# Kernel tuning notes

Measured on AMD Instinct MI355X. Metric: run time of the kernel, lower is better.

Reference implementation:

```python
import jax, jax.numpy as jnp
import numpy as np

NUM_NODES = 100000
NUM_EDGES = 1600000
EMB, HID, IN = 32, 64, 128


def gcn_conv(x, W, b, src, dst, n):
    # PyG GCNConv: add self-loops, symmetric normalization, linear transform, sum-aggregate, bias.
    h = x @ W                                   # [n, out]
    deg = jnp.zeros((n,), x.dtype).at[dst].add(1.0) + 1.0  # degree incl. self-loop
    dinv = jax.lax.rsqrt(deg)                   # deg^{-1/2}
    norm = dinv[src] * dinv[dst]                # [E]
    msg = h[src] * norm[:, None]                # gather + scale  [E, out]
    agg = jax.ops.segment_sum(msg, dst, num_segments=n)
    agg = agg + h * (dinv * dinv)[:, None]      # self-loop contribution
    return agg + b


def setup_inputs() -> dict:
    key = jax.random.key(0)
    ks = jax.random.split(key, 10)
    f32 = jnp.float32
    edge_index = jax.random.randint(ks[0], (2, NUM_EDGES), 0, NUM_NODES, dtype=jnp.int64 if jax.config.jax_enable_x64 else jnp.int32)
    def glorot(k, fan_in, fan_out):
        s = (6.0 / (fan_in + fan_out)) ** 0.5
        return jax.random.uniform(k, (fan_in, fan_out), f32, -s, s)
    return {
        'edge_index': edge_index,
        'embedding': jax.random.normal(ks[1], (NUM_NODES, EMB), f32),
        'We1': glorot(ks[2], EMB, HID), 'be1': jnp.zeros((HID,), f32),
        'We2': glorot(ks[3], HID, EMB), 'be2': jnp.zeros((EMB,), f32),
        'Wd1': glorot(ks[4], EMB, HID), 'bd1': jnp.zeros((HID,), f32),
        'Wd2': glorot(ks[5], HID, IN),  'bd2': jnp.zeros((IN,), f32),
    }


def reference(edge_index, embedding, We1, be1, We2, be2, Wd1, bd1, Wd2, bd2):
    src, dst = edge_index[0], edge_index[1]
    n = NUM_NODES
    # encoder
    x = jax.nn.relu(gcn_conv(embedding, We1, be1, src, dst, n))
    z = jax.nn.relu(gcn_conv(x, We2, be2, src, dst, n))
    # decoder
    y = jax.nn.relu(gcn_conv(z, Wd1, bd1, src, dst, n))
    recon_x = gcn_conv(y, Wd2, bd2, src, dst, n)
    return (recon_x, z)
```

## Files before the change

kernel.cpp:

```cpp
#include <hip/hip_runtime.h>
#include <hip/hip_fp16.h>

#define NN 100000
#define NE 1600000
#define NB 782
#define EPB 8192
#define NBLK_A 196
#define SCNT (NB * NBLK_A)
#define SC_NB ((SCNT + 1023) / 1024)
#define CAP 4096


__global__ void bhistA_kernel(const int* __restrict__ dst, int* __restrict__ histT) {
    __shared__ int hist[NB];
    int t = threadIdx.x, b = blockIdx.x;
    for (int i = t; i < NB; i += 256) hist[i] = 0;
    __syncthreads();
    int e0 = b * EPB;
    for (int i = t; i < EPB; i += 256) {
        int e = e0 + i;
        if (e < NE) atomicAdd(&hist[dst[e] >> 7], 1);
    }
    __syncthreads();
    for (int i = t; i < NB; i += 256) histT[i * NBLK_A + b] = hist[i];
}

__global__ void scan1g_kernel(const int* __restrict__ in, int* __restrict__ out,
                              int* __restrict__ blkSum) {
    __shared__ int ts[256];
    int t = threadIdx.x, b = blockIdx.x;
    int base = b * 1024 + t * 4;
    int4 c = {0, 0, 0, 0};
    if (base < SCNT) c = *(const int4*)(in + base);
    int s = c.x + c.y + c.z + c.w;
    ts[t] = s;
    __syncthreads();
    for (int ofs = 1; ofs < 256; ofs <<= 1) {
        int v = (t >= ofs) ? ts[t - ofs] : 0;
        __syncthreads();
        ts[t] += v;
        __syncthreads();
    }
    if (t == 255) blkSum[b] = ts[255];
    int ex = ts[t] - s;
    if (base < SCNT) {
        int4 p;
        p.x = ex; p.y = ex + c.x; p.z = p.y + c.y; p.w = p.z + c.z;
        *(int4*)(out + base) = p;
    }
}

__global__ void scan2g_kernel(int* __restrict__ blkSum) {
    __shared__ int ts[256];
    int t = threadIdx.x;
    int v = (t < SC_NB) ? blkSum[t] : 0;
    ts[t] = v;
    __syncthreads();
    for (int ofs = 1; ofs < 256; ofs <<= 1) {
        int u = (t >= ofs) ? ts[t - ofs] : 0;
        __syncthreads();
        ts[t] += u;
        __syncthreads();
    }
    if (t < SC_NB) blkSum[t] = ts[t] - v;
}

__global__ void scan3g_kernel(int* __restrict__ out, const int* __restrict__ blkSum) {
    int b = blockIdx.x;
    int base = b * 1024 + threadIdx.x * 4;
    int off = blkSum[b];
    if (base < SCNT) {
        int4 p = *(const int4*)(out + base);
        p.x += off; p.y += off; p.z += off; p.w += off;
        *(int4*)(out + base) = p;
    }
}

__global__ void bscatB_kernel(const int* __restrict__ src, const int* __restrict__ dst,
                              const int* __restrict__ scanT, int2* __restrict__ ebuf) {
    __shared__ int cur[NB];
    int t = threadIdx.x, b = blockIdx.x;
    for (int i = t; i < NB; i += 256) cur[i] = scanT[i * NBLK_A + b];
    __syncthreads();
    int e0 = b * EPB;
    for (int i = t; i < EPB; i += 256) {
        int e = e0 + i;
        if (e < NE) {
            int d = dst[e];
            int p = atomicAdd(&cur[d >> 7], 1);
            ebuf[p] = make_int2(src[e], d);
        }
    }
}

__global__ void csrC_kernel(const int2* __restrict__ ebuf, const int* __restrict__ scanT,
                            int* __restrict__ row_ptr, int* __restrict__ col,
                            float* __restrict__ dinv) {
    __shared__ int2 es[CAP];
    __shared__ int hist[128];
    __shared__ int ts[128];
    __shared__ int cur[128];
    int t = threadIdx.x, b = blockIdx.x;
    int base = scanT[b * NBLK_A];
    int end  = (b + 1 < NB) ? scanT[(b + 1) * NBLK_A] : NE;
    int cnt = end - base;
    if (t < 128) hist[t] = 0;
    __syncthreads();
    for (int i = t; i < cnt; i += 256) {
        int2 e = ebuf[base + i];
        if (i < CAP) es[i] = e;
        atomicAdd(&hist[e.y & 127], 1);
    }
    __syncthreads();
    if (t < 128) ts[t] = hist[t];
    __syncthreads();
    for (int ofs = 1; ofs < 128; ofs <<= 1) {
        int v = 0;
        if (t < 128 && t >= ofs) v = ts[t - ofs];
        __syncthreads();
        if (t < 128) ts[t] += v;
        __syncthreads();
    }
    if (t < 128) {
        int ex = ts[t] - hist[t];
        cur[t] = ex;
        int g = b * 128 + t;
        if (g < NN) {
            row_ptr[g] = base + ex;
            dinv[g] = rsqrtf((float)hist[t] + 1.0f);
        }
    }
    if (b == 0 && t == 0) row_ptr[NN] = NE;
    __syncthreads();
    for (int i = t; i < cnt; i += 256) {
        int2 e = (i < CAP) ? es[i] : ebuf[base + i];
        int r = atomicAdd(&cur[e.y & 127], 1);
        col[base + r] = e.x;
    }
}


__device__ inline ushort4 f4_to_h4(float4 v) {
    ushort4 o;
    o.x = __half_as_ushort(__float2half(v.x));
    o.y = __half_as_ushort(__float2half(v.y));
    o.z = __half_as_ushort(__float2half(v.z));
    o.w = __half_as_ushort(__float2half(v.w));
    return o;
}

template<int C>
__global__ void quant_kernel(const float4* __restrict__ x, const float* __restrict__ dinv,
                             ushort4* __restrict__ q) {
    constexpr int TPN = C / 4;
    int gid = blockIdx.x * blockDim.x + threadIdx.x;
    if (gid >= NN * TPN) return;
    int node = gid / TPN;
    float d = dinv[node];
    float4 v = x[gid];
    v.x *= d; v.y *= d; v.z *= d; v.w *= d;
    q[gid] = f4_to_h4(v);
}

template<int IN, int OUT, bool RELU, bool HASBIAS, bool QUANT>
__global__ void mm_kernel(const float* __restrict__ x, const float* __restrict__ W,
                          const float* __restrict__ bias, const float* __restrict__ dinv,
                          float4* __restrict__ out, ushort4* __restrict__ qout) {
    constexpr int CG   = OUT / 4;
    constexpr int RG   = 256 / CG;
    constexpr int ROWS = RG * 4;
    constexpr int P    = IN + 4;
    __shared__ float4 Ws[IN * CG];
    __shared__ float  xs[ROWS * P];

    int tid = threadIdx.x;
    const float4* W4 = (const float4*)W;
    for (int i = tid; i < IN * CG; i += 256) Ws[i] = W4[i];

    int n0 = blockIdx.x * ROWS;
    for (int i = tid; i < ROWS * IN; i += 256) {
        int r = i / IN, c = i & (IN - 1);
        size_t g = (size_t)n0 * IN + i;
        if (g < (size_t)NN * IN) xs[r * P + c] = x[g];
    }
    __syncthreads();

    int cg = tid % CG;
    int rg = tid / CG;

    float4 acc[4] = {{0,0,0,0},{0,0,0,0},{0,0,0,0},{0,0,0,0}};
#pragma unroll 2
    for (int k = 0; k < IN; k += 4) {
        float4 w0 = Ws[(k + 0) * CG + cg];
        float4 w1 = Ws[(k + 1) * CG + cg];
        float4 w2 = Ws[(k + 2) * CG + cg];
        float4 w3 = Ws[(k + 3) * CG + cg];
#pragma unroll
        for (int i = 0; i < 4; ++i) {
            float4 xq = *(const float4*)&xs[(i * RG + rg) * P + k];
            acc[i].x = fmaf(xq.x, w0.x, acc[i].x);
            acc[i].y = fmaf(xq.x, w0.y, acc[i].y);
            acc[i].z = fmaf(xq.x, w0.z, acc[i].z);
            acc[i].w = fmaf(xq.x, w0.w, acc[i].w);
            acc[i].x = fmaf(xq.y, w1.x, acc[i].x);
            acc[i].y = fmaf(xq.y, w1.y, acc[i].y);
            acc[i].z = fmaf(xq.y, w1.z, acc[i].z);
            acc[i].w = fmaf(xq.y, w1.w, acc[i].w);
            acc[i].x = fmaf(xq.z, w2.x, acc[i].x);
            acc[i].y = fmaf(xq.z, w2.y, acc[i].y);
            acc[i].z = fmaf(xq.z, w2.z, acc[i].z);
            acc[i].w = fmaf(xq.z, w2.w, acc[i].w);
            acc[i].x = fmaf(xq.w, w3.x, acc[i].x);
            acc[i].y = fmaf(xq.w, w3.y, acc[i].y);
            acc[i].z = fmaf(xq.w, w3.z, acc[i].z);
            acc[i].w = fmaf(xq.w, w3.w, acc[i].w);
        }
    }

    float4 bb = {0, 0, 0, 0};
    if (HASBIAS) bb = ((const float4*)bias)[cg];
#pragma unroll
    for (int i = 0; i < 4; ++i) {
        int node = n0 + i * RG + rg;
        if (node >= NN) continue;
        float4 r = acc[i];
        if (HASBIAS) { r.x += bb.x; r.y += bb.y; r.z += bb.z; r.w += bb.w; }
        if (RELU) {
            r.x = fmaxf(r.x, 0.f); r.y = fmaxf(r.y, 0.f);
            r.z = fmaxf(r.z, 0.f); r.w = fmaxf(r.w, 0.f);
        }
        if (QUANT) {
            float d = dinv[node];
            r.x *= d; r.y *= d; r.z *= d; r.w *= d;
            qout[(size_t)node * CG + cg] = f4_to_h4(r);
        } else {
            out[(size_t)node * CG + cg] = r;
        }
    }
}


__device__ inline void acc8(float* a, uint4 u) {
    const __half2* hp = (const __half2*)&u;
#pragma unroll
    for (int q = 0; q < 4; ++q) {
        float2 f = __half22float2(hp[q]);
        a[2 * q]     += f.x;
        a[2 * q + 1] += f.y;
    }
}

template<int C, bool BIASRELU, bool WRITE_Q>
__global__ void agg_kernel(const uint4* __restrict__ h, const int* __restrict__ row_ptr,
                           const int* __restrict__ col, const float* __restrict__ dinv,
                           const float* __restrict__ b, float4* __restrict__ out,
                           uint4* __restrict__ qout) {
    constexpr int TPN = C / 8;
    int gid = blockIdx.x * blockDim.x + threadIdx.x;
    int node = gid / TPN;
    int cg = gid % TPN;
    if (node >= NN) return;
    int beg = row_ptr[node];
    int end = row_ptr[node + 1];

    float a[8] = {0, 0, 0, 0, 0, 0, 0, 0};
    acc8(a, h[(size_t)node * TPN + cg]);

    int j = beg;
    for (; j + 4 <= end; j += 4) {
        int s0 = col[j], s1 = col[j + 1], s2 = col[j + 2], s3 = col[j + 3];
        uint4 u0 = h[(size_t)s0 * TPN + cg];
        uint4 u1 = h[(size_t)s1 * TPN + cg];
        uint4 u2 = h[(size_t)s2 * TPN + cg];
        uint4 u3 = h[(size_t)s3 * TPN + cg];
        acc8(a, u0); acc8(a, u1); acc8(a, u2); acc8(a, u3);
    }
    for (; j < end; ++j) acc8(a, h[(size_t)col[j] * TPN + cg]);

    float d = dinv[node];
    float r[8];
    if (BIASRELU) {
        const float* bp = b + cg * 8;
#pragma unroll
        for (int q = 0; q < 8; ++q) r[q] = fmaxf(fmaf(d, a[q], bp[q]), 0.f);
    } else {
#pragma unroll
        for (int q = 0; q < 8; ++q) r[q] = d * a[q];
    }
    float4* op = out + (size_t)node * (C / 4) + cg * 2;
    op[0] = make_float4(r[0], r[1], r[2], r[3]);
    op[1] = make_float4(r[4], r[5], r[6], r[7]);
    if (WRITE_Q) {
        uint4 qv;
        __half2* qp = (__half2*)&qv;
#pragma unroll
        for (int q = 0; q < 4; ++q)
            qp[q] = __float22half2_rn(make_float2(r[2 * q] * d, r[2 * q + 1] * d));
        qout[(size_t)node * TPN + cg] = qv;
    }
}


extern "C" void kernel_launch(void* const* d_in, const int* in_sizes, int n_in,
                              void* d_out, int out_size, void* d_ws, size_t ws_size,
                              hipStream_t stream) {
    const int* ei = (const int*)d_in[0];
    const int* src = ei;
    const int* dst = ei + NE;
    const float* emb = (const float*)d_in[1];
    const float* We1 = (const float*)d_in[2]; const float* be1 = (const float*)d_in[3];
    const float* We2 = (const float*)d_in[4]; const float* be2 = (const float*)d_in[5];
    const float* Wd1 = (const float*)d_in[6]; const float* bd1 = (const float*)d_in[7];
    const float* Wd2 = (const float*)d_in[8]; const float* bd2 = (const float*)d_in[9];

    float* outp  = (float*)d_out;
    float* recon = outp;
    float* z     = outp + (size_t)NN * 128;

    char* ws = (char*)d_ws;
    size_t off = 0;
    auto alloc = [&](size_t bytes) {
        void* p = ws + off;
        off += (bytes + 255) & ~(size_t)255;
        return p;
    };
    int*     row_ptr = (int*)    alloc((size_t)(NN + 1) * 4);
    int*     col     = (int*)    alloc((size_t)NE * 4);
    float*   dinv    = (float*)  alloc((size_t)NN * 4);
    int*     histT   = (int*)    alloc((size_t)SCNT * 4);
    int*     scanT   = (int*)    alloc((size_t)SCNT * 4);
    int*     blkSum  = (int*)    alloc((size_t)SC_NB * 4);
    void*    region1 = alloc((size_t)NE * 8);
    ushort4* qA      = (ushort4*)alloc((size_t)NN * 64 * 2);
    ushort4* qB      = (ushort4*)alloc((size_t)NN * 64 * 2);
    float*   fB      = (float*)  alloc((size_t)NN * 64 * 4);
    int2*    ebuf    = (int2*)region1;
    float*   fA      = (float*)region1;
    (void)ws_size; (void)in_sizes; (void)n_in; (void)out_size;

    bhistA_kernel<<<NBLK_A, 256, 0, stream>>>(dst, histT);
    scan1g_kernel<<<SC_NB, 256, 0, stream>>>(histT, scanT, blkSum);
    scan2g_kernel<<<1, 256, 0, stream>>>(blkSum);
    scan3g_kernel<<<SC_NB, 256, 0, stream>>>(scanT, blkSum);
    bscatB_kernel<<<NBLK_A, 256, 0, stream>>>(src, dst, scanT, ebuf);
    csrC_kernel<<<NB, 256, 0, stream>>>(ebuf, scanT, row_ptr, col, dinv);

    quant_kernel<32><<<(NN * 8 + 255) / 256, 256, 0, stream>>>((const float4*)emb, dinv, qA);
    agg_kernel<32, false, false><<<(NN * 4 + 255) / 256, 256, 0, stream>>>(
        (const uint4*)qA, row_ptr, col, dinv, nullptr, (float4*)fA, nullptr);
    mm_kernel<32, 64, true, true, false><<<(NN + 63) / 64, 256, 0, stream>>>(
        fA, We1, be1, dinv, (float4*)fB, nullptr);

    mm_kernel<64, 32, false, false, true><<<(NN + 127) / 128, 256, 0, stream>>>(
        fB, We2, nullptr, dinv, nullptr, qB);
    agg_kernel<32, true, true><<<(NN * 4 + 255) / 256, 256, 0, stream>>>(
        (const uint4*)qB, row_ptr, col, dinv, be2, (float4*)z, (uint4*)qA);

    agg_kernel<32, false, false><<<(NN * 4 + 255) / 256, 256, 0, stream>>>(
        (const uint4*)qA, row_ptr, col, dinv, nullptr, (float4*)fA, nullptr);
    mm_kernel<32, 64, true, true, true><<<(NN + 63) / 64, 256, 0, stream>>>(
        fA, Wd1, bd1, dinv, nullptr, qB);

    agg_kernel<64, false, false><<<(NN * 8 + 255) / 256, 256, 0, stream>>>(
        (const uint4*)qB, row_ptr, col, dinv, nullptr, (float4*)fB, nullptr);
    mm_kernel<64, 128, false, true, false><<<(NN + 31) / 32, 256, 0, stream>>>(
        fB, Wd2, bd2, dinv, (float4*)recon, nullptr);
}
```

Baseline: 260.2 us.

## Pack edge bucket entries into one int, add blocks, unroll gathers by eight

Edges in the bucket buffer are now packed into a single 32-bit word, with the source in the low 20 bits and the local destination row in the high bits, instead of an int2. This halves the scatter and CSR-build traffic and the shared-memory staging footprint. The histogram and scatter passes use four times more blocks with fewer edges each, which grows the transposed histogram, so the second scan stage moves to 1024 threads. The aggregation kernel gains an 8-wide gather loop to keep more loads in flight, at the cost of more registers.

```diff
diff --git a/kernel.cpp b/kernel.cpp
--- a/kernel.cpp
+++ b/kernel.cpp
@@ -4,8 +4,8 @@
 #define NN 100000
 #define NE 1600000
 #define NB 782
-#define EPB 8192
-#define NBLK_A 196
+#define EPB 2048
+#define NBLK_A 782
 #define SCNT (NB * NBLK_A)
 #define SC_NB ((SCNT + 1023) / 1024)
 #define CAP 4096
@@ -51,12 +51,12 @@
 }
 
 __global__ void scan2g_kernel(int* __restrict__ blkSum) {
-    __shared__ int ts[256];
+    __shared__ int ts[1024];
     int t = threadIdx.x;
     int v = (t < SC_NB) ? blkSum[t] : 0;
     ts[t] = v;
     __syncthreads();
-    for (int ofs = 1; ofs < 256; ofs <<= 1) {
+    for (int ofs = 1; ofs < 1024; ofs <<= 1) {
         int u = (t >= ofs) ? ts[t - ofs] : 0;
         __syncthreads();
         ts[t] += u;
@@ -77,7 +77,7 @@
 }
 
 __global__ void bscatB_kernel(const int* __restrict__ src, const int* __restrict__ dst,
-                              const int* __restrict__ scanT, int2* __restrict__ ebuf) {
+                              const int* __restrict__ scanT, int* __restrict__ ebuf) {
     __shared__ int cur[NB];
     int t = threadIdx.x, b = blockIdx.x;
     for (int i = t; i < NB; i += 256) cur[i] = scanT[i * NBLK_A + b];
@@ -88,15 +88,15 @@
         if (e < NE) {
             int d = dst[e];
             int p = atomicAdd(&cur[d >> 7], 1);
-            ebuf[p] = make_int2(src[e], d);
-        }
-    }
-}
-
-__global__ void csrC_kernel(const int2* __restrict__ ebuf, const int* __restrict__ scanT,
+            ebuf[p] = src[e] | ((d & 127) << 20);
+        }
+    }
+}
+
+__global__ void csrC_kernel(const int* __restrict__ ebuf, const int* __restrict__ scanT,
                             int* __restrict__ row_ptr, int* __restrict__ col,
                             float* __restrict__ dinv) {
-    __shared__ int2 es[CAP];
+    __shared__ int es[CAP];
     __shared__ int hist[128];
     __shared__ int ts[128];
     __shared__ int cur[128];
@@ -107,9 +107,9 @@
     if (t < 128) hist[t] = 0;
     __syncthreads();
     for (int i = t; i < cnt; i += 256) {
-        int2 e = ebuf[base + i];
+        int e = ebuf[base + i];
         if (i < CAP) es[i] = e;
-        atomicAdd(&hist[e.y & 127], 1);
+        atomicAdd(&hist[e >> 20], 1);
     }
     __syncthreads();
     if (t < 128) ts[t] = hist[t];
@@ -133,9 +133,9 @@
     if (b == 0 && t == 0) row_ptr[NN] = NE;
     __syncthreads();
     for (int i = t; i < cnt; i += 256) {
-        int2 e = (i < CAP) ? es[i] : ebuf[base + i];
-        int r = atomicAdd(&cur[e.y & 127], 1);
-        col[base + r] = e.x;
+        int e = (i < CAP) ? es[i] : ebuf[base + i];
+        int r = atomicAdd(&cur[e >> 20], 1);
+        col[base + r] = e & 0xFFFFF;
     }
 }
 
@@ -267,6 +267,16 @@
     acc8(a, h[(size_t)node * TPN + cg]);
 
     int j = beg;
+    for (; j + 8 <= end; j += 8) {
+        int s[8];
+        uint4 u[8];
+#pragma unroll
+        for (int q = 0; q < 8; ++q) s[q] = col[j + q];
+#pragma unroll
+        for (int q = 0; q < 8; ++q) u[q] = h[(size_t)s[q] * TPN + cg];
+#pragma unroll
+        for (int q = 0; q < 8; ++q) acc8(a, u[q]);
+    }
     for (; j + 4 <= end; j += 4) {
         int s0 = col[j], s1 = col[j + 1], s2 = col[j + 2], s3 = col[j + 3];
         uint4 u0 = h[(size_t)s0 * TPN + cg];
@@ -330,17 +340,17 @@
     int*     histT   = (int*)    alloc((size_t)SCNT * 4);
     int*     scanT   = (int*)    alloc((size_t)SCNT * 4);
     int*     blkSum  = (int*)    alloc((size_t)SC_NB * 4);
-    void*    region1 = alloc((size_t)NE * 8);
+    void*    region1 = alloc((size_t)NN * 32 * 4);
     ushort4* qA      = (ushort4*)alloc((size_t)NN * 64 * 2);
     ushort4* qB      = (ushort4*)alloc((size_t)NN * 64 * 2);
     float*   fB      = (float*)  alloc((size_t)NN * 64 * 4);
-    int2*    ebuf    = (int2*)region1;
+    int*     ebuf    = (int*)region1;
     float*   fA      = (float*)region1;
     (void)ws_size; (void)in_sizes; (void)n_in; (void)out_size;
 
     bhistA_kernel<<<NBLK_A, 256, 0, stream>>>(dst, histT);
     scan1g_kernel<<<SC_NB, 256, 0, stream>>>(histT, scanT, blkSum);
-    scan2g_kernel<<<1, 256, 0, stream>>>(blkSum);
+    scan2g_kernel<<<1, 1024, 0, stream>>>(blkSum);
     scan3g_kernel<<<SC_NB, 256, 0, stream>>>(scanT, blkSum);
     bscatB_kernel<<<NBLK_A, 256, 0, stream>>>(src, dst, scanT, ebuf);
     csrC_kernel<<<NB, 256, 0, stream>>>(ebuf, scanT, row_ptr, col, dinv);
```

After: 259.5 us. About the same (-0.3%).
